# Kernel tuning notes

Hardware: AMD Instinct MI355X
Metric: run time of the kernel (lower is better)

Reference implementation:

```python
import jax, jax.numpy as jnp
import numpy as np
from jax import lax


def conv(x, w, b, stride, pad):
    # x: [B,C,H,W], w: [O,I,kh,kw] (torch layout)
    y = lax.conv_general_dilated(x, w, (stride, stride), ((pad, pad), (pad, pad)),
                                 dimension_numbers=('NCHW', 'OIHW', 'NCHW'))
    return y + b[None, :, None, None]


def convT(x, w, b, stride, pad):
    # torch ConvTranspose2d weight layout [in, out, kh, kw]
    k = w.shape[2]
    wf = jnp.flip(w, (2, 3)).transpose(1, 0, 2, 3)  # -> [out, in, kh, kw]
    p = k - 1 - pad
    y = lax.conv_general_dilated(x, wf, (1, 1), ((p, p), (p, p)),
                                 lhs_dilation=(stride, stride),
                                 dimension_numbers=('NCHW', 'OIHW', 'NCHW'))
    return y + b[None, :, None, None]


def resblock(x, wa, ba, wb, bb):
    h = conv(jax.nn.relu(x), wa, ba, 1, 1)   # 3x3
    h2 = conv(jax.nn.relu(h), wb, bb, 1, 0)  # 1x1
    return x + h2


def vqvae_forward(x, e1_w, e1_b, e2_w, e2_b, e3_w, e3_b,
                  er1a_w, er1a_b, er1b_w, er1b_b, er2a_w, er2a_b, er2b_w, er2b_b,
                  codebook,
                  d1_w, d1_b, dr1a_w, dr1a_b, dr1b_w, dr1b_b,
                  dr2a_w, dr2a_b, dr2b_w, dr2b_b,
                  dt1_w, dt1_b, dt2_w, dt2_b):
    # encoder
    h = jax.nn.relu(conv(x, e1_w, e1_b, 2, 1))
    h = jax.nn.relu(conv(h, e2_w, e2_b, 2, 1))
    h = conv(h, e3_w, e3_b, 1, 1)
    h = resblock(h, er1a_w, er1a_b, er1b_w, er1b_b)
    ze = resblock(h, er2a_w, er2a_b, er2b_w, er2b_b)  # [B,C,H,W]
    # VQ: nearest codebook vector per spatial location (squared L2)
    zef = ze.transpose(0, 2, 3, 1)  # [B,H,W,C]
    # ||z - e||^2 = ||z||^2 - 2 z.e + ||e||^2 (same argmin as explicit broadcast)
    d = (jnp.sum(zef * zef, -1, keepdims=True)
         - 2.0 * jnp.einsum('bhwc,kc->bhwk', zef, codebook)
         + jnp.sum(codebook * codebook, -1))  # [B,H,W,K]
    idx = jnp.argmin(d, -1)                    # [B,H,W]
    zq = codebook[idx].transpose(0, 3, 1, 2)   # [B,C,H,W]
    # straight-through estimator
    dec_in = ze + lax.stop_gradient(zq - ze)
    # decoder
    g = conv(dec_in, d1_w, d1_b, 1, 1)
    g = resblock(g, dr1a_w, dr1a_b, dr1b_w, dr1b_b)
    g = resblock(g, dr2a_w, dr2a_b, dr2b_w, dr2b_b)
    g = jax.nn.relu(convT(g, dt1_w, dt1_b, 2, 1))
    x_hat = convT(g, dt2_w, dt2_b, 2, 1)
    return x_hat, ze, zq


def setup_inputs() -> dict:
    key = jax.random.key(0)
    ks = iter(jax.random.split(key, 64))
    C, K = 128, 512

    def w(shape, scale=0.02):
        return jax.random.normal(next(ks), shape, jnp.float32) * scale

    inp = {}
    inp['x'] = jax.random.normal(next(ks), (16, 3, 256, 256), jnp.float32)
    inp['e1_w'] = w((C, 3, 4, 4)); inp['e1_b'] = w((C,))
    inp['e2_w'] = w((C, C, 4, 4)); inp['e2_b'] = w((C,))
    inp['e3_w'] = w((C, C, 3, 3)); inp['e3_b'] = w((C,))
    inp['er1a_w'] = w((C, C, 3, 3)); inp['er1a_b'] = w((C,))
    inp['er1b_w'] = w((C, C, 1, 1)); inp['er1b_b'] = w((C,))
    inp['er2a_w'] = w((C, C, 3, 3)); inp['er2a_b'] = w((C,))
    inp['er2b_w'] = w((C, C, 1, 1)); inp['er2b_b'] = w((C,))
    inp['codebook'] = jax.random.uniform(next(ks), (K, C), jnp.float32, -1.0 / K, 1.0 / K)
    inp['d1_w'] = w((C, C, 3, 3)); inp['d1_b'] = w((C,))
    inp['dr1a_w'] = w((C, C, 3, 3)); inp['dr1a_b'] = w((C,))
    inp['dr1b_w'] = w((C, C, 1, 1)); inp['dr1b_b'] = w((C,))
    inp['dr2a_w'] = w((C, C, 3, 3)); inp['dr2a_b'] = w((C,))
    inp['dr2b_w'] = w((C, C, 1, 1)); inp['dr2b_b'] = w((C,))
    inp['dt1_w'] = w((C, C, 4, 4)); inp['dt1_b'] = w((C,))   # ConvTranspose [in,out,kh,kw]
    inp['dt2_w'] = w((C, 3, 4, 4)); inp['dt2_b'] = w((3,))
    return inp


def reference(x, e1_w, e1_b, e2_w, e2_b, e3_w, e3_b,
              er1a_w, er1a_b, er1b_w, er1b_b, er2a_w, er2a_b, er2b_w, er2b_b,
              codebook,
              d1_w, d1_b, dr1a_w, dr1a_b, dr1b_w, dr1b_b,
              dr2a_w, dr2a_b, dr2b_w, dr2b_b,
              dt1_w, dt1_b, dt2_w, dt2_b):
    return vqvae_forward(x, e1_w, e1_b, e2_w, e2_b, e3_w, e3_b,
                         er1a_w, er1a_b, er1b_w, er1b_b, er2a_w, er2a_b, er2b_w, er2b_b,
                         codebook,
                         d1_w, d1_b, dr1a_w, dr1a_b, dr1b_w, dr1b_b,
                         dr2a_w, dr2a_b, dr2b_w, dr2b_b,
                         dt1_w, dt1_b, dt2_w, dt2_b)
```

## Files before the change

### kernel.cpp

```cpp
#include <hip/hip_runtime.h>
#include <stdint.h>

typedef unsigned short u16;
typedef __attribute__((ext_vector_type(8))) short short8;
typedef __attribute__((ext_vector_type(4))) float floatx4;

#define RS66  (66*128)
#define IS66  (66*66*128)
#define RS130 (130*128)
#define IS130 (130*130*128)

__device__ __forceinline__ float bf2f(u16 h) {
  union { unsigned u; float f; } v; v.u = ((unsigned)h) << 16; return v.f;
}
__device__ __forceinline__ u16 f2bf(float f) {
  union { float f; unsigned u; } v; v.f = f;
  unsigned r = v.u + 0x7FFFu + ((v.u >> 16) & 1u);
  return (u16)(r >> 16);
}
__device__ __forceinline__ void gl_lds16(const void* g, void* l) {
  __builtin_amdgcn_global_load_lds(
      (const __attribute__((address_space(1))) void*)(uintptr_t)g,
      (__attribute__((address_space(3))) void*)(uintptr_t)l, 16, 0, 0);
}
__device__ __forceinline__ unsigned fkey(float f) {
  unsigned u = __float_as_uint(f);
  return (u & 0x80000000u) ? ~u : (u | 0x80000000u);
}

struct Taps { int n; unsigned dh2; unsigned dw2; };

__global__ __launch_bounds__(256, 3) void conv_mfma(
    const u16* __restrict__ in, int inRS, int inIS, int si,
    const u16* __restrict__ wt, const float* __restrict__ bias, Taps tp,
    u16* __restrict__ out, int outRS, int outIS, int so, int oh0, int ow0,
    const u16* __restrict__ res, u16* __restrict__ out2, int reluMain,
    float* __restrict__ zeFc, u16* __restrict__ zeBFc, int multi)
{
  __shared__ u16 lA[2][8192];
  const int tid = threadIdx.x;
  const int w = tid >> 6, lane = tid & 63, quad = lane >> 4, l16 = lane & 15;
  const int wm = w >> 1, wn = w & 1;
  const int bx = ((blockIdx.x & 7) << 6) | (blockIdx.x >> 3);
  const int blockM = bx << 7;

  unsigned dh2 = tp.dh2, dw2 = tp.dw2;
  if (multi) {
    const int cls = blockIdx.y;
    dh2 = (tp.dh2 >> (8*cls)) & 0xffu;
    dw2 = (tp.dw2 >> (8*cls)) & 0xffu;
    wt += cls << 16;
    oh0 = cls >> 1; ow0 = cls & 1;
  }

  const int swz = (tid & 7) ^ ((tid >> 3) & 7);
  const u16* gA[4];
#pragma unroll
  for (int i=0;i<4;i++) {
    const int pg = blockM + i*32 + (tid >> 3);
    const int b = pg >> 12, mo = (pg >> 6) & 63, no = pg & 63;
    gA[i] = in + b*inIS + si*mo*inRS + si*no*128 + swz*8;
  }
  const u16* gBf = wt + (wn*64 + l16)*32 + quad*8;
  const int ldsOff = w*512;

  floatx4 zz = {0.f,0.f,0.f,0.f};
  floatx4 acc[4][4];
#pragma unroll
  for (int i=0;i<4;i++)
#pragma unroll
    for (int j=0;j<4;j++) acc[i][j] = zz;

  auto issueA = [&](int ci, int buf) {
    const int t = ci >> 1, kc = ci & 1;
    const int dh = (int)((dh2 >> (2*t)) & 3u) - 1;
    const int dw = (int)((dw2 >> (2*t)) & 3u) - 1;
    const int aoff = dh*inRS + dw*128 + kc*64;
#pragma unroll
    for (int i=0;i<4;i++)
      gl_lds16(gA[i] + aoff, &lA[buf][i*2048 + ldsOff]);
  };
  short8 bX[4], bY[4];
  auto loadB = [&](int ci, int kk, short8 (&b)[4]) {
    const u16* p = gBf + ci*8192 + kk*4096;
#pragma unroll
    for (int s=0;s<4;s++) b[s] = *(const short8*)(p + s*512);
  };
  auto computeH = [&](const u16* bufA, int kk, short8 (&bfr)[4]) {
    short8 af[4];
#pragma unroll
    for (int s=0;s<4;s++) {
      const int row = wm*64 + s*16 + l16;
      af[s] = *(const short8*)&bufA[row*64 + (((kk*4 + quad) ^ (l16 & 7)) << 3)];
    }
#pragma unroll
    for (int i=0;i<4;i++)
#pragma unroll
      for (int j=0;j<4;j++)
        acc[i][j] = __builtin_amdgcn_mfma_f32_16x16x32_bf16(af[i], bfr[j], acc[i][j], 0, 0, 0);
  };

  const int NCH = tp.n << 1;
  loadB(0, 0, bX);
  issueA(0, 0);
  for (int ci = 0; ci < NCH; ++ci) {
    __syncthreads();
    if (ci + 1 < NCH) issueA(ci + 1, (ci + 1) & 1);
    const u16* bufA = lA[ci & 1];
    loadB(ci, 1, bY);
    computeH(bufA, 0, bX);
    if (ci + 1 < NCH) loadB(ci + 1, 0, bX);
    computeH(bufA, 1, bY);
  }

  float bv[4];
#pragma unroll
  for (int j=0;j<4;j++) bv[j] = bias[wn*64 + j*16 + l16];

#pragma unroll
  for (int i=0;i<4;i++) {
#pragma unroll
    for (int r=0;r<4;r++) {
      const int p = blockM + wm*64 + i*16 + quad*4 + r;
      const int bb = p >> 12, mo = (p >> 6) & 63, no = p & 63;
      const int ob = bb*outIS + (so*mo + oh0)*outRS + (so*no + ow0)*128;
#pragma unroll
      for (int j=0;j<4;j++) {
        const int n = wn*64 + j*16 + l16;
        float v = acc[i][j][r] + bv[j];
        if (res)  v += bf2f(res[ob + n]);
        if (out)  out[ob + n]  = f2bf(reluMain ? fmaxf(v, 0.f) : v);
        if (out2) out2[ob + n] = f2bf(fmaxf(v, 0.f));
        if (zeFc) {
          zeFc[((size_t)p << 7) + n] = v;
          zeBFc[((size_t)p << 7) + n] = f2bf(v);
        }
      }
    }
  }
}

__global__ __launch_bounds__(256, 3) void vq_score(
    const u16* __restrict__ zeBF, const u16* __restrict__ cbF,
    const float* __restrict__ cbn, unsigned long long* __restrict__ minbuf)
{
  __shared__ u16 lA[2][8192];
  const int tid = threadIdx.x;
  const int w = tid >> 6, lane = tid & 63, quad = lane >> 4, l16 = lane & 15;
  const int wm = w >> 1, wn = w & 1;
  const int bx = ((blockIdx.x & 7) << 6) | (blockIdx.x >> 3);
  const int blockM = bx << 7;
  const int nb = blockIdx.y;
  const int swz = (tid & 7) ^ ((tid >> 3) & 7);
  const u16* gA[4];
#pragma unroll
  for (int i=0;i<4;i++)
    gA[i] = zeBF + ((size_t)(blockM + i*32 + (tid >> 3)) << 7) + swz*8;
  const u16* gBf = cbF + (nb << 14) + (wn*64 + l16)*32 + quad*8;
  const int ldsOff = w*512;

  floatx4 zz = {0.f,0.f,0.f,0.f};
  floatx4 acc[4][4];
#pragma unroll
  for (int i=0;i<4;i++)
#pragma unroll
    for (int j=0;j<4;j++) acc[i][j] = zz;

  auto issueA = [&](int kc, int buf) {
#pragma unroll
    for (int i=0;i<4;i++)
      gl_lds16(gA[i] + kc*64, &lA[buf][i*2048 + ldsOff]);
  };
  short8 bX[4], bY[4];
  auto loadB = [&](int ci, int kk, short8 (&b)[4]) {
    const u16* p = gBf + ci*8192 + kk*4096;
#pragma unroll
    for (int s=0;s<4;s++) b[s] = *(const short8*)(p + s*512);
  };
  auto computeH = [&](const u16* bufA, int kk, short8 (&bfr)[4]) {
    short8 af[4];
#pragma unroll
    for (int s=0;s<4;s++) {
      const int row = wm*64 + s*16 + l16;
      af[s] = *(const short8*)&bufA[row*64 + (((kk*4 + quad) ^ (l16 & 7)) << 3)];
    }
#pragma unroll
    for (int i=0;i<4;i++)
#pragma unroll
      for (int j=0;j<4;j++)
        acc[i][j] = __builtin_amdgcn_mfma_f32_16x16x32_bf16(af[i], bfr[j], acc[i][j], 0, 0, 0);
  };

  loadB(0, 0, bX);
  issueA(0, 0);
  for (int ci = 0; ci < 2; ++ci) {
    __syncthreads();
    if (ci == 0) issueA(1, 1);
    const u16* bufA = lA[ci];
    loadB(ci, 1, bY);
    computeH(bufA, 0, bX);
    if (ci == 0) loadB(1, 0, bX);
    computeH(bufA, 1, bY);
  }

  float cn[4];
#pragma unroll
  for (int j=0;j<4;j++) cn[j] = cbn[nb*128 + wn*64 + j*16 + l16];

#pragma unroll
  for (int i=0;i<4;i++) {
#pragma unroll
    for (int r=0;r<4;r++) {
      const int p = blockM + wm*64 + i*16 + quad*4 + r;
      unsigned long long best = 0xFFFFFFFFFFFFFFFFull;
#pragma unroll
      for (int j=0;j<4;j++) {
        const int n = nb*128 + wn*64 + j*16 + l16;
        float v = cn[j] - acc[i][j][r];
        unsigned long long pk = ((unsigned long long)fkey(v) << 32) | (unsigned)n;
        if (pk < best) best = pk;
      }
#pragma unroll
      for (int d=1; d<16; d<<=1) {
        unsigned long long o = __shfl_xor(best, d, 64);
        if (o < best) best = o;
      }
      if (l16 == 0) atomicMin(minbuf + p, best);
    }
  }
}

__global__ __launch_bounds__(256) void finalize(
    const float* __restrict__ zeFc, const unsigned long long* __restrict__ minb,
    const float* __restrict__ cb, float* __restrict__ outZe, float* __restrict__ outZq,
    u16* __restrict__ zqI)
{
  __shared__ float T[64*129];
  __shared__ int ns[64];
  const int tid = threadIdx.x;
  const int P0 = blockIdx.x << 6;
  const int b = P0 >> 12, hw0 = P0 & 4095;

#pragma unroll
  for (int it=0; it<32; ++it) {
    int e = it*256 + tid;
    int px = e >> 7, c = e & 127;
    T[px*129 + c] = zeFc[((size_t)P0 << 7) + e];
  }
  if (tid < 64) ns[tid] = (int)(unsigned)(minb[P0 + tid] & 0xFFFFFFFFull);
  __syncthreads();

  float* zeB = outZe + (((size_t)b) << 19) + hw0;
  float* zqB = outZq + (((size_t)b) << 19) + hw0;
  const int h = hw0 >> 6;
  u16* zqIB = zqI + b*IS66 + h*RS66;
#pragma unroll
  for (int it=0; it<32; ++it) {
    const int c = it*4 + (tid >> 6);
    const int px = tid & 63;
    zeB[(c << 12) + px] = T[px*129 + c];
    float v = cb[(ns[px] << 7) + c];
    zqB[(c << 12) + px] = v;
    zqIB[px*128 + c] = f2bf(v);
  }
}

__global__ __launch_bounds__(256) void zero_halos(
    u16* big, u16* s0, u16* s1, u16* s2, u16* s3, unsigned long long* minb)
{
  int id = blockIdx.x*256 + threadIdx.x;
  if (id >= 463872) return;
  if (id >= 398336) { minb[id - 398336] = 0xFFFFFFFFFFFFFFFFull; return; }
  u16* base; int H, W;
  if (id < 132096) { base = big; H = 128; W = 128; }
  else {
    id -= 132096;
    int bi = id / 66560;
    id -= bi*66560;
    base = (bi == 0) ? s0 : (bi == 1) ? s1 : (bi == 2) ? s2 : s3;
    H = 64; W = 64;
  }
  int Wp = W+2, Hp = H+2;
  int cv = id & 15; int rest = id >> 4;
  int npx = 2*Wp + 2*H;
  int img = rest / npx; int pix = rest - img*npx;
  int hh, wwp;
  if (pix < Wp) { hh = 0; wwp = pix; }
  else if (pix < 2*Wp) { hh = Hp-1; wwp = pix - Wp; }
  else { int r2 = pix - 2*Wp; hh = 1 + (r2 >> 1); wwp = (r2 & 1) ? (Wp-1) : 0; }
  uint4 zv = {0u,0u,0u,0u};
  *(uint4*)(base + (((size_t)img*Hp + hh)*Wp + wwp)*128 + cv*8) = zv;
}

struct WEnt { const float* src; u16* dst; int O, I, T, mode; };
struct WTab { int n; WEnt e[16]; int cum[17]; };
__global__ __launch_bounds__(256) void prep_w(WTab wt) {
  int id = blockIdx.x*256 + threadIdx.x;
  if (id >= wt.cum[wt.n]) return;
  int k = 0;
  while (id >= wt.cum[k+1]) k++;
  int l = id - wt.cum[k];
  WEnt E = wt.e[k];
  if (E.mode == 6) {
    int e = l & 7, quad = (l >> 3) & 3, row = (l >> 5) & 127;
    int kk = (l >> 12) & 1, kc = (l >> 13) & 1, t = l >> 14;
    int i = kc*64 + kk*32 + quad*8 + e;
    E.dst[l] = f2bf(E.src[(row*E.I + i)*E.T + t]);
  } else if (E.mode == 1) {
    int e = l & 7, quad = (l >> 3) & 3, row = (l >> 5) & 127;
    int kk = (l >> 12) & 1, kc = (l >> 13) & 1, tt = (l >> 14) & 3, cls = l >> 16;
    int i = kc*64 + kk*32 + quad*8 + e;
    int th = tt >> 1, tw = tt & 1, po = cls >> 1, pw = cls & 1;
    int kh = po ? (th ? 2 : 0) : (th ? 3 : 1);
    int kw = pw ? (tw ? 2 : 0) : (tw ? 3 : 1);
    E.dst[l] = f2bf(E.src[((i*128 + row)*4 + kh)*4 + kw]);
  } else if (E.mode == 7) {
    int e = l & 7, quad = (l >> 3) & 3, row = (l >> 5) & 127;
    int kk = (l >> 12) & 1, kc = (l >> 13) & 1, tt = l >> 14;
    int i = kc*64 + kk*32 + quad*8 + e;
    E.dst[l] = f2bf(E.src[(tt*128 + row)*128 + i]);
  } else if (E.mode == 3) {
    float s = 0.f; const float* r = E.src + l*128;
    for (int c=0;c<128;c++) s += r[c]*r[c];
    ((float*)E.dst)[l] = 0.5f*s;
  } else if (E.mode == 4) {
    int o = l & 127, tap = l >> 7;
    ((float*)E.dst)[l] = E.src[o*48 + tap];
  } else {
    int c = l & 127, n = l >> 7;
    int o = n >> 4, kk = n & 15;
    E.dst[l] = f2bf(E.src[c*48 + o*16 + kk]);
  }
}

__global__ __launch_bounds__(256) void conv_e1(
    const float* __restrict__ x, const float* __restrict__ wT,
    const float* __restrict__ bias, u16* __restrict__ outI)
{
  __shared__ float inS[12*260];
  __shared__ float wS[48*128];
  __shared__ float bS[128];
  const int tid = threadIdx.x;
  const int b = blockIdx.x >> 7, ho = blockIdx.x & 127;

  for (int l = tid; l < 1536; l += 256)
    ((float4*)wS)[l] = ((const float4*)wT)[l];
  if (tid < 128) bS[tid] = bias[tid];
  for (int l = tid; l < 3120; l += 256) {
    int col = l % 260; int rest = l / 260;
    int kh = rest & 3, c = rest >> 2;
    int hi = 2*ho + kh - 1, wi = col - 1;
    float v = 0.f;
    if ((unsigned)hi < 256u && (unsigned)wi < 256u)
      v = x[((b*3 + c) << 16) + (hi << 8) + wi];
    inS[rest*260 + col] = v;
  }
  __syncthreads();

  const int g = tid & 7;
  const int pxg = tid >> 3;
  floatx4 acc[4][4];
  {
    const floatx4* bp = (const floatx4*)&bS[g*16];
    floatx4 b0 = bp[0], b1 = bp[1], b2 = bp[2], b3 = bp[3];
#pragma unroll
    for (int px=0;px<4;px++) { acc[px][0]=b0; acc[px][1]=b1; acc[px][2]=b2; acc[px][3]=b3; }
  }
#pragma unroll
  for (int c=0;c<3;c++)
#pragma unroll
    for (int kh=0;kh<4;kh++) {
      const float* row = &inS[(c*4+kh)*260];
#pragma unroll
      for (int kw=0;kw<4;kw++) {
        const int tap = c*16 + kh*4 + kw;
        const floatx4* wp = (const floatx4*)&wS[tap*128 + g*16];
        floatx4 w0 = wp[0], w1 = wp[1], w2 = wp[2], w3 = wp[3];
#pragma unroll
        for (int px=0;px<4;px++) {
          float xv = row[((pxg*4 + px) << 1) + kw];
          acc[px][0] += xv*w0; acc[px][1] += xv*w1;
          acc[px][2] += xv*w2; acc[px][3] += xv*w3;
        }
      }
    }

  u16* ob = outI + b*IS130 + ho*RS130;
#pragma unroll
  for (int px=0;px<4;px++) {
    const int wo = pxg*4 + px;
    u16* p = ob + wo*128 + g*16;
#pragma unroll
    for (int k=0;k<4;k++) {
      union { u16 u[4]; uint2 v2; } pk;
#pragma unroll
      for (int j=0;j<4;j++) pk.u[j] = f2bf(fmaxf(acc[px][k][j], 0.f));
      *(uint2*)(p + k*4) = pk.v2;
    }
  }
}

__global__ __launch_bounds__(256) void dt2_gemm(
    const u16* __restrict__ inI, const u16* __restrict__ Wb,
    float* __restrict__ cols)
{
  const int tid = threadIdx.x;
  const int w = tid >> 6, lane = tid & 63, quad = lane >> 4, l16 = lane & 15;
  const int pixBase = blockIdx.x*256 + w*64;

  short8 Bf[3][4];
#pragma unroll
  for (int nt=0; nt<3; nt++)
#pragma unroll
    for (int kc=0; kc<4; kc++)
      Bf[nt][kc] = *(const short8*)(Wb + (nt*16 + l16)*128 + kc*32 + quad*8);

  const u16* ap[4];
#pragma unroll
  for (int ms=0; ms<4; ms++) {
    int p = pixBase + ms*16 + l16;
    int b = p >> 14, rem = p & 16383;
    ap[ms] = inI + b*IS130 + (rem >> 7)*RS130 + (rem & 127)*128;
  }

  floatx4 zz = {0.f,0.f,0.f,0.f};
  floatx4 acc[4][3];
#pragma unroll
  for (int ms=0; ms<4; ms++)
#pragma unroll
    for (int nt=0; nt<3; nt++) acc[ms][nt] = zz;

#pragma unroll
  for (int kc=0; kc<4; kc++) {
#pragma unroll
    for (int ms=0; ms<4; ms++) {
      short8 a = *(const short8*)(ap[ms] + kc*32 + quad*8);
#pragma unroll
      for (int nt=0; nt<3; nt++)
        acc[ms][nt] = __builtin_amdgcn_mfma_f32_16x16x32_bf16(a, Bf[nt][kc], acc[ms][nt], 0, 0, 0);
    }
  }

#pragma unroll
  for (int ms=0; ms<4; ms++)
#pragma unroll
    for (int nt=0; nt<3; nt++)
#pragma unroll
      for (int r=0; r<4; r++) {
        int p = pixBase + ms*16 + quad*4 + r;
        cols[(size_t)p*48 + nt*16 + l16] = acc[ms][nt][r];
      }
}

__global__ __launch_bounds__(256) void dt2_gather(
    const float* __restrict__ cols, const float* __restrict__ bias,
    float* __restrict__ xhat)
{
  int id = blockIdx.x*256 + threadIdx.x;
  int b = id >> 16, rem = id & 65535;
  int ho = rem >> 8, wo = rem & 255;
  const int ph = ho & 1, pw = wo & 1;
  const int hi0 = ph ? ((ho+1)>>1) : (ho>>1);
  const int kh0 = ph ? 0 : 1;
  const int wi0 = pw ? ((wo+1)>>1) : (wo>>1);
  const int kw0 = pw ? 0 : 1;
  float a0 = bias[0], a1 = bias[1], a2 = bias[2];
#pragma unroll
  for (int th=0; th<2; th++) {
    const int hi = hi0 - th;
    if ((unsigned)hi >= 128u) continue;
    const int kh = kh0 + 2*th;
#pragma unroll
    for (int tw=0; tw<2; tw++) {
      const int wi = wi0 - tw;
      if ((unsigned)wi >= 128u) continue;
      const int kw = kw0 + 2*tw;
      const float* r = cols + (size_t)((b << 14) + (hi << 7) + wi)*48 + (kh*4 + kw);
      a0 += r[0]; a1 += r[16]; a2 += r[32];
    }
  }
  const int ob = ((b*3) << 16) + (ho << 8) + wo;
  xhat[ob]          = a0;
  xhat[ob + 65536]  = a1;
  xhat[ob + 131072] = a2;
}

extern "C" void kernel_launch(void* const* d_in, const int* in_sizes, int n_in,
                              void* d_out, int out_size, void* d_ws, size_t ws_size,
                              hipStream_t stream)
{
  const float* x     = (const float*)d_in[0];
  const float* e1w   = (const float*)d_in[1];
  const float* e1b   = (const float*)d_in[2];
  const float* e2w   = (const float*)d_in[3];
  const float* e2b   = (const float*)d_in[4];
  const float* e3w   = (const float*)d_in[5];
  const float* e3b   = (const float*)d_in[6];
  const float* er1aw = (const float*)d_in[7];
  const float* er1ab = (const float*)d_in[8];
  const float* er1bw = (const float*)d_in[9];
  const float* er1bb = (const float*)d_in[10];
  const float* er2aw = (const float*)d_in[11];
  const float* er2ab = (const float*)d_in[12];
  const float* er2bw = (const float*)d_in[13];
  const float* er2bb = (const float*)d_in[14];
  const float* cb    = (const float*)d_in[15];
  const float* d1w   = (const float*)d_in[16];
  const float* d1b   = (const float*)d_in[17];
  const float* dr1aw = (const float*)d_in[18];
  const float* dr1ab = (const float*)d_in[19];
  const float* dr1bw = (const float*)d_in[20];
  const float* dr1bb = (const float*)d_in[21];
  const float* dr2aw = (const float*)d_in[22];
  const float* dr2ab = (const float*)d_in[23];
  const float* dr2bw = (const float*)d_in[24];
  const float* dr2bb = (const float*)d_in[25];
  const float* dt1w  = (const float*)d_in[26];
  const float* dt1b  = (const float*)d_in[27];
  const float* dt2w  = (const float*)d_in[28];
  const float* dt2b  = (const float*)d_in[29];
  float* out = (float*)d_out;

  char* ws = (char*)d_ws;
  size_t off = 0;
  auto alloc = [&](size_t bytes) -> void* {
    void* r = ws + off; off += (bytes + 255) & ~(size_t)255; return r;
  };

  u16* BIG = (u16*)alloc((size_t)IS130*16*2);
  u16* S[4];
  for (int i=0;i<4;i++) S[i] = (u16*)alloc((size_t)IS66*16*2);
  unsigned long long* minb = (unsigned long long*)alloc((size_t)65536*8);
  u16* W_e2 = (u16*)alloc(262144*2);
  u16* W9[6]; for (int i=0;i<6;i++) W9[i] = (u16*)alloc(147456*2);
  u16* W1[4]; for (int i=0;i<4;i++) W1[i] = (u16*)alloc(16384*2);
  u16* Wdt1 = (u16*)alloc(262144*2);
  u16* cbBF = (u16*)alloc(65536*2);
  float* cbn = (float*)alloc(512*4);
  float* wsE1 = (float*)alloc(6144*4);
  u16* Wb48 = (u16*)alloc(6144*2);

  u16* BIGi = BIG + RS130 + 128;
  u16* Si[4];
  for (int i=0;i<4;i++) Si[i] = S[i] + RS66 + 128;
  u16* zeBFc = S[1];
  float* zeFc = (float*)BIG;
  float* cols = (float*)S[1];

  zero_halos<<<1812, 256, 0, stream>>>(BIG, S[0], S[1], S[2], S[3], minb);

  WTab wtab; int ne = 0; wtab.cum[0] = 0;
  auto addw = [&](const float* s, u16* d, int O, int I, int T, int m, int items) {
    wtab.e[ne] = {s, d, O, I, T, m};
    wtab.cum[ne+1] = wtab.cum[ne] + items; ne++;
  };
  addw(e2w,   W_e2, 128,128,16,6, 262144);
  addw(e3w,   W9[0],128,128, 9,6, 147456);
  addw(er1aw, W9[1],128,128, 9,6, 147456);
  addw(er2aw, W9[2],128,128, 9,6, 147456);
  addw(d1w,   W9[3],128,128, 9,6, 147456);
  addw(dr1aw, W9[4],128,128, 9,6, 147456);
  addw(dr2aw, W9[5],128,128, 9,6, 147456);
  addw(er1bw, W1[0],128,128, 1,6, 16384);
  addw(er2bw, W1[1],128,128, 1,6, 16384);
  addw(dr1bw, W1[2],128,128, 1,6, 16384);
  addw(dr2bw, W1[3],128,128, 1,6, 16384);
  addw(dt1w,  Wdt1, 0,0,0,1, 262144);
  addw(cb,    cbBF, 0,0,0,7, 65536);
  addw(cb,    (u16*)cbn, 0,0,0,3, 512);
  addw(e1w,   (u16*)wsE1, 0,0,0,4, 6144);
  addw(dt2w,  Wb48, 0,0,0,5, 6144);
  wtab.n = ne;
  prep_w<<<(wtab.cum[ne] + 255)/256, 256, 0, stream>>>(wtab);

  conv_e1<<<2048, 256, 0, stream>>>(x, wsE1, e1b, BIGi);

  Taps t16; t16.n = 16; t16.dh2 = 0; t16.dw2 = 0;
  for (int t=0;t<16;t++) { t16.dh2 |= (unsigned)(t>>2) << (2*t); t16.dw2 |= (unsigned)(t&3) << (2*t); }
  Taps t9; t9.n = 9; t9.dh2 = 0; t9.dw2 = 0;
  for (int t=0;t<9;t++) { t9.dh2 |= (unsigned)(t/3) << (2*t); t9.dw2 |= (unsigned)(t%3) << (2*t); }
  Taps t1x; t1x.n = 1; t1x.dh2 = 1; t1x.dw2 = 1;
  Taps tcm; tcm.n = 4; tcm.dh2 = 0; tcm.dw2 = 0;
  for (int cls=0; cls<4; ++cls) {
    int po = cls >> 1, pw = cls & 1;
    for (int tt=0; tt<4; ++tt) {
      int th = tt >> 1, tw = tt & 1;
      int dh = po ? (th ? 0 : 1) : (th ? -1 : 0);
      int dw = pw ? (tw ? 0 : 1) : (tw ? -1 : 0);
      tcm.dh2 |= (unsigned)(dh+1) << (8*cls + 2*tt);
      tcm.dw2 |= (unsigned)(dw+1) << (8*cls + 2*tt);
    }
  }

  auto conv = [&](const u16* in_, int iRS, int iIS, int si,
                  const u16* w_, const float* b_, Taps tp,
                  u16* o_, int oRS, int oIS, int so, int oh, int ow,
                  const u16* r_, u16* o2, int rl, float* zf, u16* zb) {
    conv_mfma<<<512, 256, 0, stream>>>(in_, iRS, iIS, si, w_, b_, tp,
                                       o_, oRS, oIS, so, oh, ow, r_, o2, rl, zf, zb, 0);
  };

  conv(BIGi, RS130, IS130, 2, W_e2, e2b, t16, Si[0], RS66, IS66, 1,0,0, nullptr, nullptr, 1, nullptr, nullptr);
  conv(Si[0], RS66, IS66, 1, W9[0], e3b, t9, Si[1], RS66, IS66, 1,0,0, nullptr, Si[2], 0, nullptr, nullptr);
  conv(Si[2], RS66, IS66, 1, W9[1], er1ab, t9, Si[0], RS66, IS66, 1,0,0, nullptr, nullptr, 1, nullptr, nullptr);
  conv(Si[0], RS66, IS66, 1, W1[0], er1bb, t1x, Si[3], RS66, IS66, 1,0,0, Si[1], Si[2], 0, nullptr, nullptr);
  conv(Si[2], RS66, IS66, 1, W9[2], er2ab, t9, Si[0], RS66, IS66, 1,0,0, nullptr, nullptr, 1, nullptr, nullptr);
  conv(Si[0], RS66, IS66, 1, W1[1], er2bb, t1x, nullptr, RS66, IS66, 1,0,0, Si[3], nullptr, 0, zeFc, zeBFc);

  vq_score<<<dim3(512,4), 256, 0, stream>>>(zeBFc, cbBF, cbn, minb);
  finalize<<<1024, 256, 0, stream>>>(zeFc, minb, cb, out + 3145728, out + 11534336, Si[2]);

  conv(Si[2], RS66, IS66, 1, W9[3], d1b, t9, Si[0], RS66, IS66, 1,0,0, nullptr, Si[1], 0, nullptr, nullptr);
  conv(Si[1], RS66, IS66, 1, W9[4], dr1ab, t9, Si[2], RS66, IS66, 1,0,0, nullptr, nullptr, 1, nullptr, nullptr);
  conv(Si[2], RS66, IS66, 1, W1[2], dr1bb, t1x, Si[3], RS66, IS66, 1,0,0, Si[0], Si[1], 0, nullptr, nullptr);
  conv(Si[1], RS66, IS66, 1, W9[5], dr2ab, t9, Si[2], RS66, IS66, 1,0,0, nullptr, nullptr, 1, nullptr, nullptr);
  conv(Si[2], RS66, IS66, 1, W1[3], dr2bb, t1x, Si[0], RS66, IS66, 1,0,0, Si[3], nullptr, 0, nullptr, nullptr);

  conv_mfma<<<dim3(512,4), 256, 0, stream>>>(Si[0], RS66, IS66, 1, Wdt1, dt1b, tcm,
                                             BIGi, RS130, IS130, 2, 0, 0,
                                             nullptr, nullptr, 1, nullptr, nullptr, 1);

  dt2_gemm<<<1024, 256, 0, stream>>>(BIGi, Wb48, cols);
  dt2_gather<<<4096, 256, 0, stream>>>(cols, dt2b, out);
}
```

Measured before the change: 730.4 us.

## Replace direct global-to-LDS loads with register-staged triple-buffered LDS pipeline

The conv and VQ-score MFMA kernels stop using global_load_lds and instead load A tiles into registers, then write them to LDS with a swizzled ds_write. The conv main loop gains a third LDS buffer and is unrolled by two, so global loads for chunk ci+2 and B-fragment loads for ci+1 are in flight while the current chunk is computed. The plain __syncthreads is replaced by an lgkmcnt wait plus s_barrier and sched_barrier. This adds register pressure (extra A and B fragment arrays) and 50% more LDS per block, which may cut occupancy under launch_bounds(256,3).

```diff
diff --git a/kernel.cpp b/kernel.cpp
--- a/kernel.cpp
+++ b/kernel.cpp
@@ -18,14 +18,14 @@
   unsigned r = v.u + 0x7FFFu + ((v.u >> 16) & 1u);
   return (u16)(r >> 16);
 }
-__device__ __forceinline__ void gl_lds16(const void* g, void* l) {
-  __builtin_amdgcn_global_load_lds(
-      (const __attribute__((address_space(1))) void*)(uintptr_t)g,
-      (__attribute__((address_space(3))) void*)(uintptr_t)l, 16, 0, 0);
-}
 __device__ __forceinline__ unsigned fkey(float f) {
   unsigned u = __float_as_uint(f);
   return (u & 0x80000000u) ? ~u : (u | 0x80000000u);
+}
+__device__ __forceinline__ void lgkmbar() {
+  asm volatile("s_waitcnt lgkmcnt(0)" ::: "memory");
+  __builtin_amdgcn_s_barrier();
+  __builtin_amdgcn_sched_barrier(0);
 }
 
 struct Taps { int n; unsigned dh2; unsigned dw2; };
@@ -37,7 +37,7 @@
     const u16* __restrict__ res, u16* __restrict__ out2, int reluMain,
     float* __restrict__ zeFc, u16* __restrict__ zeBFc, int multi)
 {
-  __shared__ u16 lA[2][8192];
+  __shared__ u16 lA[3][8192];
   const int tid = threadIdx.x;
   const int w = tid >> 6, lane = tid & 63, quad = lane >> 4, l16 = lane & 15;
   const int wm = w >> 1, wn = w & 1;
@@ -54,15 +54,15 @@
   }
 
   const int swz = (tid & 7) ^ ((tid >> 3) & 7);
+  const int wOff = (tid >> 3)*64 + swz*8;
   const u16* gA[4];
 #pragma unroll
   for (int i=0;i<4;i++) {
     const int pg = blockM + i*32 + (tid >> 3);
     const int b = pg >> 12, mo = (pg >> 6) & 63, no = pg & 63;
-    gA[i] = in + b*inIS + si*mo*inRS + si*no*128 + swz*8;
+    gA[i] = in + b*inIS + si*mo*inRS + si*no*128 + (tid & 7)*8;
   }
   const u16* gBf = wt + (wn*64 + l16)*32 + quad*8;
-  const int ldsOff = w*512;
 
   floatx4 zz = {0.f,0.f,0.f,0.f};
   floatx4 acc[4][4];
@@ -71,27 +71,31 @@
 #pragma unroll
     for (int j=0;j<4;j++) acc[i][j] = zz;
 
-  auto issueA = [&](int ci, int buf) {
+  auto gloadA = [&](int ci, short8 (&a)[4]) {
     const int t = ci >> 1, kc = ci & 1;
     const int dh = (int)((dh2 >> (2*t)) & 3u) - 1;
     const int dw = (int)((dw2 >> (2*t)) & 3u) - 1;
     const int aoff = dh*inRS + dw*128 + kc*64;
 #pragma unroll
-    for (int i=0;i<4;i++)
-      gl_lds16(gA[i] + aoff, &lA[buf][i*2048 + ldsOff]);
-  };
-  short8 bX[4], bY[4];
-  auto loadB = [&](int ci, int kk, short8 (&b)[4]) {
-    const u16* p = gBf + ci*8192 + kk*4096;
-#pragma unroll
-    for (int s=0;s<4;s++) b[s] = *(const short8*)(p + s*512);
-  };
-  auto computeH = [&](const u16* bufA, int kk, short8 (&bfr)[4]) {
+    for (int i=0;i<4;i++) a[i] = *(const short8*)(gA[i] + aoff);
+  };
+  auto dswA = [&](u16* P, short8 (&a)[4]) {
+#pragma unroll
+    for (int i=0;i<4;i++) *(short8*)(P + i*2048 + wOff) = a[i];
+  };
+  auto loadB = [&](int ci, short8 (&k0)[4], short8 (&k1)[4]) {
+    const u16* p = gBf + ci*8192;
+#pragma unroll
+    for (int s=0;s<4;s++) k0[s] = *(const short8*)(p + s*512);
+#pragma unroll
+    for (int s=0;s<4;s++) k1[s] = *(const short8*)(p + 4096 + s*512);
+  };
+  auto computeH = [&](const u16* P, int kk, short8 (&bfr)[4]) {
     short8 af[4];
 #pragma unroll
     for (int s=0;s<4;s++) {
       const int row = wm*64 + s*16 + l16;
-      af[s] = *(const short8*)&bufA[row*64 + (((kk*4 + quad) ^ (l16 & 7)) << 3)];
+      af[s] = *(const short8*)&P[row*64 + (((kk*4 + quad) ^ (l16 & 7)) << 3)];
     }
 #pragma unroll
     for (int i=0;i<4;i++)
@@ -101,16 +105,30 @@
   };
 
   const int NCH = tp.n << 1;
-  loadB(0, 0, bX);
-  issueA(0, 0);
-  for (int ci = 0; ci < NCH; ++ci) {
-    __syncthreads();
-    if (ci + 1 < NCH) issueA(ci + 1, (ci + 1) & 1);
-    const u16* bufA = lA[ci & 1];
-    loadB(ci, 1, bY);
-    computeH(bufA, 0, bX);
-    if (ci + 1 < NCH) loadB(ci + 1, 0, bX);
-    computeH(bufA, 1, bY);
+  short8 a0[4], a1[4], bA0[4], bB0[4], bA1[4], bB1[4];
+  gloadA(0, a0);
+  gloadA(1, a1);
+  loadB(0, bA0, bB0);
+  u16 *Pc = &lA[0][0], *Pn = &lA[1][0], *Pw = &lA[2][0];
+  dswA(Pc, a0);
+
+  for (int ci = 0; ci < NCH; ci += 2) {
+    dswA(Pn, a1);
+    if (ci + 2 < NCH) gloadA(ci + 2, a0);
+    loadB(ci + 1, bA1, bB1);
+    lgkmbar();
+    computeH(Pc, 0, bA0);
+    computeH(Pc, 1, bB0);
+    { u16* t = Pc; Pc = Pn; Pn = Pw; Pw = t; }
+    if (ci + 2 < NCH) {
+      dswA(Pn, a0);
+      if (ci + 3 < NCH) gloadA(ci + 3, a1);
+      loadB(ci + 2, bA0, bB0);
+      lgkmbar();
+    }
+    computeH(Pc, 0, bA1);
+    computeH(Pc, 1, bB1);
+    { u16* t = Pc; Pc = Pn; Pn = Pw; Pw = t; }
   }
 
   float bv[4];
@@ -122,8 +140,8 @@
 #pragma unroll
     for (int r=0;r<4;r++) {
       const int p = blockM + wm*64 + i*16 + quad*4 + r;
-      const int bb = p >> 12, mo = (p >> 6) & 63, no = p & 63;
-      const int ob = bb*outIS + (so*mo + oh0)*outRS + (so*no + ow0)*128;
+      const int bb2 = p >> 12, mo = (p >> 6) & 63, no = p & 63;
+      const int ob = bb2*outIS + (so*mo + oh0)*outRS + (so*no + ow0)*128;
 #pragma unroll
       for (int j=0;j<4;j++) {
         const int n = wn*64 + j*16 + l16;
@@ -152,12 +170,12 @@
   const int blockM = bx << 7;
   const int nb = blockIdx.y;
   const int swz = (tid & 7) ^ ((tid >> 3) & 7);
+  const int wOff = (tid >> 3)*64 + swz*8;
   const u16* gA[4];
 #pragma unroll
   for (int i=0;i<4;i++)
-    gA[i] = zeBF + ((size_t)(blockM + i*32 + (tid >> 3)) << 7) + swz*8;
+    gA[i] = zeBF + ((size_t)(blockM + i*32 + (tid >> 3)) << 7) + (tid & 7)*8;
   const u16* gBf = cbF + (nb << 14) + (wn*64 + l16)*32 + quad*8;
-  const int ldsOff = w*512;
 
   floatx4 zz = {0.f,0.f,0.f,0.f};
   floatx4 acc[4][4];
@@ -166,23 +184,27 @@
 #pragma unroll
     for (int j=0;j<4;j++) acc[i][j] = zz;
 
-  auto issueA = [&](int kc, int buf) {
-#pragma unroll
-    for (int i=0;i<4;i++)
-      gl_lds16(gA[i] + kc*64, &lA[buf][i*2048 + ldsOff]);
-  };
-  short8 bX[4], bY[4];
-  auto loadB = [&](int ci, int kk, short8 (&b)[4]) {
-    const u16* p = gBf + ci*8192 + kk*4096;
-#pragma unroll
-    for (int s=0;s<4;s++) b[s] = *(const short8*)(p + s*512);
-  };
-  auto computeH = [&](const u16* bufA, int kk, short8 (&bfr)[4]) {
+  auto gloadA = [&](int ci, short8 (&a)[4]) {
+#pragma unroll
+    for (int i=0;i<4;i++) a[i] = *(const short8*)(gA[i] + ci*64);
+  };
+  auto dswA = [&](u16* P, short8 (&a)[4]) {
+#pragma unroll
+    for (int i=0;i<4;i++) *(short8*)(P + i*2048 + wOff) = a[i];
+  };
+  auto loadB = [&](int ci, short8 (&k0)[4], short8 (&k1)[4]) {
+    const u16* p = gBf + ci*8192;
+#pragma unroll
+    for (int s=0;s<4;s++) k0[s] = *(const short8*)(p + s*512);
+#pragma unroll
+    for (int s=0;s<4;s++) k1[s] = *(const short8*)(p + 4096 + s*512);
+  };
+  auto computeH = [&](const u16* P, int kk, short8 (&bfr)[4]) {
     short8 af[4];
 #pragma unroll
     for (int s=0;s<4;s++) {
       const int row = wm*64 + s*16 + l16;
-      af[s] = *(const short8*)&bufA[row*64 + (((kk*4 + quad) ^ (l16 & 7)) << 3)];
+      af[s] = *(const short8*)&P[row*64 + (((kk*4 + quad) ^ (l16 & 7)) << 3)];
     }
 #pragma unroll
     for (int i=0;i<4;i++)
@@ -191,17 +213,20 @@
         acc[i][j] = __builtin_amdgcn_mfma_f32_16x16x32_bf16(af[i], bfr[j], acc[i][j], 0, 0, 0);
   };
 
-  loadB(0, 0, bX);
-  issueA(0, 0);
-  for (int ci = 0; ci < 2; ++ci) {
-    __syncthreads();
-    if (ci == 0) issueA(1, 1);
-    const u16* bufA = lA[ci];
-    loadB(ci, 1, bY);
-    computeH(bufA, 0, bX);
-    if (ci == 0) loadB(1, 0, bX);
-    computeH(bufA, 1, bY);
-  }
+  short8 a0[4], a1[4], bA0[4], bB0[4], bA1[4], bB1[4];
+  gloadA(0, a0);
+  gloadA(1, a1);
+  loadB(0, bA0, bB0);
+  loadB(1, bA1, bB1);
+  u16 *P0 = &lA[0][0], *P1 = &lA[1][0];
+  dswA(P0, a0);
+  lgkmbar();
+  computeH(P0, 0, bA0);
+  computeH(P0, 1, bB0);
+  dswA(P1, a1);
+  lgkmbar();
+  computeH(P1, 0, bA1);
+  computeH(P1, 1, bB1);
 
   float cn[4];
 #pragma unroll
```

Measured after the change: 1.194 ms. 1.64x slower.

## Load conv GEMM A-operand directly from global into registers, drop LDS staging

Applied to the files above, without the earlier changes.

Replaces the LDS double-buffered A tile (global_load_lds plus syncthreads) in conv_mfma and vq_score with direct per-lane global loads of A and B fragments into registers. A four-deep register pipeline of A/B fragments overlaps loads with MFMA work, and launch bounds drop to 2 blocks per CU to make room for the extra registers. This removes barriers and LDS traffic, but each wave now fetches its own A rows with no sharing across waves, so global/L2 traffic for A doubles and occupancy drops.

```diff
diff --git a/kernel.cpp b/kernel.cpp
--- a/kernel.cpp
+++ b/kernel.cpp
@@ -18,11 +18,6 @@
   unsigned r = v.u + 0x7FFFu + ((v.u >> 16) & 1u);
   return (u16)(r >> 16);
 }
-__device__ __forceinline__ void gl_lds16(const void* g, void* l) {
-  __builtin_amdgcn_global_load_lds(
-      (const __attribute__((address_space(1))) void*)(uintptr_t)g,
-      (__attribute__((address_space(3))) void*)(uintptr_t)l, 16, 0, 0);
-}
 __device__ __forceinline__ unsigned fkey(float f) {
   unsigned u = __float_as_uint(f);
   return (u & 0x80000000u) ? ~u : (u | 0x80000000u);
@@ -30,14 +25,13 @@
 
 struct Taps { int n; unsigned dh2; unsigned dw2; };
 
-__global__ __launch_bounds__(256, 3) void conv_mfma(
+__global__ __launch_bounds__(256, 2) void conv_mfma(
     const u16* __restrict__ in, int inRS, int inIS, int si,
     const u16* __restrict__ wt, const float* __restrict__ bias, Taps tp,
     u16* __restrict__ out, int outRS, int outIS, int so, int oh0, int ow0,
     const u16* __restrict__ res, u16* __restrict__ out2, int reluMain,
     float* __restrict__ zeFc, u16* __restrict__ zeBFc, int multi)
 {
-  __shared__ u16 lA[2][8192];
   const int tid = threadIdx.x;
   const int w = tid >> 6, lane = tid & 63, quad = lane >> 4, l16 = lane & 15;
   const int wm = w >> 1, wn = w & 1;
@@ -53,16 +47,14 @@
     oh0 = cls >> 1; ow0 = cls & 1;
   }
 
-  const int swz = (tid & 7) ^ ((tid >> 3) & 7);
-  const u16* gA[4];
-#pragma unroll
-  for (int i=0;i<4;i++) {
-    const int pg = blockM + i*32 + (tid >> 3);
-    const int b = pg >> 12, mo = (pg >> 6) & 63, no = pg & 63;
-    gA[i] = in + b*inIS + si*mo*inRS + si*no*128 + swz*8;
-  }
-  const u16* gBf = wt + (wn*64 + l16)*32 + quad*8;
-  const int ldsOff = w*512;
+  const u16* ap[4];
+#pragma unroll
+  for (int s=0;s<4;s++) {
+    const int p = blockM + wm*64 + s*16 + l16;
+    const int b = p >> 12, mo = (p >> 6) & 63, no = p & 63;
+    ap[s] = in + b*inIS + si*mo*inRS + si*no*128 + quad*8;
+  }
+  const u16* bp = wt + (wn*64 + l16)*32 + quad*8;
 
   floatx4 zz = {0.f,0.f,0.f,0.f};
   floatx4 acc[4][4];
@@ -71,46 +63,35 @@
 #pragma unroll
     for (int j=0;j<4;j++) acc[i][j] = zz;
 
-  auto issueA = [&](int ci, int buf) {
-    const int t = ci >> 1, kc = ci & 1;
+  auto loadAB = [&](int h, short8 (&a)[4], short8 (&b)[4]) {
+    const int t = h >> 2;
     const int dh = (int)((dh2 >> (2*t)) & 3u) - 1;
     const int dw = (int)((dw2 >> (2*t)) & 3u) - 1;
-    const int aoff = dh*inRS + dw*128 + kc*64;
+    const int aoff = dh*inRS + dw*128 + (h & 3)*32;
+#pragma unroll
+    for (int s=0;s<4;s++) a[s] = *(const short8*)(ap[s] + aoff);
+    const u16* pB = bp + h*4096;
+#pragma unroll
+    for (int s=0;s<4;s++) b[s] = *(const short8*)(pB + s*512);
+  };
+  auto mm = [&](short8 (&a)[4], short8 (&b)[4]) {
 #pragma unroll
     for (int i=0;i<4;i++)
-      gl_lds16(gA[i] + aoff, &lA[buf][i*2048 + ldsOff]);
-  };
-  short8 bX[4], bY[4];
-  auto loadB = [&](int ci, int kk, short8 (&b)[4]) {
-    const u16* p = gBf + ci*8192 + kk*4096;
-#pragma unroll
-    for (int s=0;s<4;s++) b[s] = *(const short8*)(p + s*512);
-  };
-  auto computeH = [&](const u16* bufA, int kk, short8 (&bfr)[4]) {
-    short8 af[4];
-#pragma unroll
-    for (int s=0;s<4;s++) {
-      const int row = wm*64 + s*16 + l16;
-      af[s] = *(const short8*)&bufA[row*64 + (((kk*4 + quad) ^ (l16 & 7)) << 3)];
-    }
-#pragma unroll
-    for (int i=0;i<4;i++)
 #pragma unroll
       for (int j=0;j<4;j++)
-        acc[i][j] = __builtin_amdgcn_mfma_f32_16x16x32_bf16(af[i], bfr[j], acc[i][j], 0, 0, 0);
-  };
-
-  const int NCH = tp.n << 1;
-  loadB(0, 0, bX);
-  issueA(0, 0);
-  for (int ci = 0; ci < NCH; ++ci) {
-    __syncthreads();
-    if (ci + 1 < NCH) issueA(ci + 1, (ci + 1) & 1);
-    const u16* bufA = lA[ci & 1];
-    loadB(ci, 1, bY);
-    computeH(bufA, 0, bX);
-    if (ci + 1 < NCH) loadB(ci + 1, 0, bX);
-    computeH(bufA, 1, bY);
+        acc[i][j] = __builtin_amdgcn_mfma_f32_16x16x32_bf16(a[i], b[j], acc[i][j], 0, 0, 0);
+  };
+
+  const int NH = tp.n << 2;
+  short8 a0[4],b0[4],a1[4],b1[4],a2[4],b2[4],a3[4],b3[4];
+  loadAB(0, a0, b0);
+  loadAB(1, a1, b1);
+  loadAB(2, a2, b2);
+  for (int h = 0; h < NH; h += 4) {
+    mm(a0, b0); if (h+3 < NH) loadAB(h+3, a3, b3);
+    mm(a1, b1); if (h+4 < NH) loadAB(h+4, a0, b0);
+    mm(a2, b2); if (h+5 < NH) loadAB(h+5, a1, b1);
+    mm(a3, b3); if (h+6 < NH) loadAB(h+6, a2, b2);
   }
 
   float bv[4];
@@ -140,24 +121,21 @@
   }
 }
 
-__global__ __launch_bounds__(256, 3) void vq_score(
+__global__ __launch_bounds__(256, 2) void vq_score(
     const u16* __restrict__ zeBF, const u16* __restrict__ cbF,
     const float* __restrict__ cbn, unsigned long long* __restrict__ minbuf)
 {
-  __shared__ u16 lA[2][8192];
   const int tid = threadIdx.x;
   const int w = tid >> 6, lane = tid & 63, quad = lane >> 4, l16 = lane & 15;
   const int wm = w >> 1, wn = w & 1;
-  const int bx = ((blockIdx.x & 7) << 6) | (blockIdx.x >> 3);
-  const int blockM = bx << 7;
+  const int blockM = blockIdx.x << 7;
   const int nb = blockIdx.y;
-  const int swz = (tid & 7) ^ ((tid >> 3) & 7);
-  const u16* gA[4];
-#pragma unroll
-  for (int i=0;i<4;i++)
-    gA[i] = zeBF + ((size_t)(blockM + i*32 + (tid >> 3)) << 7) + swz*8;
-  const u16* gBf = cbF + (nb << 14) + (wn*64 + l16)*32 + quad*8;
-  const int ldsOff = w*512;
+
+  const u16* ap[4];
+#pragma unroll
+  for (int s=0;s<4;s++)
+    ap[s] = zeBF + ((size_t)(blockM + wm*64 + s*16 + l16) << 7) + quad*8;
+  const u16* bp = cbF + (nb << 14) + (wn*64 + l16)*32 + quad*8;
 
   floatx4 zz = {0.f,0.f,0.f,0.f};
   floatx4 acc[4][4];
@@ -166,42 +144,29 @@
 #pragma unroll
     for (int j=0;j<4;j++) acc[i][j] = zz;
 
-  auto issueA = [&](int kc, int buf) {
+  auto loadAB = [&](int h, short8 (&a)[4], short8 (&b)[4]) {
+#pragma unroll
+    for (int s=0;s<4;s++) a[s] = *(const short8*)(ap[s] + h*32);
+    const u16* pB = bp + h*4096;
+#pragma unroll
+    for (int s=0;s<4;s++) b[s] = *(const short8*)(pB + s*512);
+  };
+  auto mm = [&](short8 (&a)[4], short8 (&b)[4]) {
 #pragma unroll
     for (int i=0;i<4;i++)
-      gl_lds16(gA[i] + kc*64, &lA[buf][i*2048 + ldsOff]);
-  };
-  short8 bX[4], bY[4];
-  auto loadB = [&](int ci, int kk, short8 (&b)[4]) {
-    const u16* p = gBf + ci*8192 + kk*4096;
-#pragma unroll
-    for (int s=0;s<4;s++) b[s] = *(const short8*)(p + s*512);
-  };
-  auto computeH = [&](const u16* bufA, int kk, short8 (&bfr)[4]) {
-    short8 af[4];
-#pragma unroll
-    for (int s=0;s<4;s++) {
-      const int row = wm*64 + s*16 + l16;
-      af[s] = *(const short8*)&bufA[row*64 + (((kk*4 + quad) ^ (l16 & 7)) << 3)];
-    }
-#pragma unroll
-    for (int i=0;i<4;i++)
 #pragma unroll
       for (int j=0;j<4;j++)
-        acc[i][j] = __builtin_amdgcn_mfma_f32_16x16x32_bf16(af[i], bfr[j], acc[i][j], 0, 0, 0);
-  };
-
-  loadB(0, 0, bX);
-  issueA(0, 0);
-  for (int ci = 0; ci < 2; ++ci) {
-    __syncthreads();
-    if (ci == 0) issueA(1, 1);
-    const u16* bufA = lA[ci];
-    loadB(ci, 1, bY);
-    computeH(bufA, 0, bX);
-    if (ci == 0) loadB(1, 0, bX);
-    computeH(bufA, 1, bY);
-  }
+        acc[i][j] = __builtin_amdgcn_mfma_f32_16x16x32_bf16(a[i], b[j], acc[i][j], 0, 0, 0);
+  };
+
+  short8 a0[4],b0[4],a1[4],b1[4],a2[4],b2[4],a3[4],b3[4];
+  loadAB(0, a0, b0);
+  loadAB(1, a1, b1);
+  loadAB(2, a2, b2);
+  mm(a0, b0); loadAB(3, a3, b3);
+  mm(a1, b1);
+  mm(a2, b2);
+  mm(a3, b3);
 
   float cn[4];
 #pragma unroll
@@ -535,7 +500,7 @@
   u16* W9[6]; for (int i=0;i<6;i++) W9[i] = (u16*)alloc(147456*2);
   u16* W1[4]; for (int i=0;i<4;i++) W1[i] = (u16*)alloc(16384*2);
   u16* Wdt1 = (u16*)alloc(262144*2);
-  u16* cbBF = (u16*)alloc(65536*2);
+  u16* cbF = (u16*)alloc(65536*2);
   float* cbn = (float*)alloc(512*4);
   float* wsE1 = (float*)alloc(6144*4);
   u16* Wb48 = (u16*)alloc(6144*2);
@@ -566,7 +531,7 @@
   addw(dr1bw, W1[2],128,128, 1,6, 16384);
   addw(dr2bw, W1[3],128,128, 1,6, 16384);
   addw(dt1w,  Wdt1, 0,0,0,1, 262144);
-  addw(cb,    cbBF, 0,0,0,7, 65536);
+  addw(cb,    cbF,  0,0,0,7, 65536);
   addw(cb,    (u16*)cbn, 0,0,0,3, 512);
   addw(e1w,   (u16*)wsE1, 0,0,0,4, 6144);
   addw(dt2w,  Wb48, 0,0,0,5, 6144);
@@ -607,7 +572,7 @@
   conv(Si[2], RS66, IS66, 1, W9[2], er2ab, t9, Si[0], RS66, IS66, 1,0,0, nullptr, nullptr, 1, nullptr, nullptr);
   conv(Si[0], RS66, IS66, 1, W1[1], er2bb, t1x, nullptr, RS66, IS66, 1,0,0, Si[3], nullptr, 0, zeFc, zeBFc);
 
-  vq_score<<<dim3(512,4), 256, 0, stream>>>(zeBFc, cbBF, cbn, minb);
+  vq_score<<<dim3(512,4), 256, 0, stream>>>(zeBFc, cbF, cbn, minb);
   finalize<<<1024, 256, 0, stream>>>(zeFc, minb, cb, out + 3145728, out + 11534336, Si[2]);
 
   conv(Si[2], RS66, IS66, 1, W9[3], d1b, t9, Si[0], RS66, IS66, 1,0,0, nullptr, Si[1], 0, nullptr, nullptr);
```

After: 996.0 us. 36.4% more time.
